# Kernel optimization log

Measured on AMD Instinct MI355X. Metric: run time of the kernel, lower is better.

The kernel has to match this reference:

```python
import jax, jax.numpy as jnp
import numpy as np

D_MODEL = 2048
NUM_HEADS = 32
NUM_KV_HEADS = 8
HEAD_DIM = D_MODEL // NUM_HEADS  # 64
KV_GROUPS = NUM_HEADS // NUM_KV_HEADS  # 4


def setup_inputs() -> dict:
    key = jax.random.key(0)
    k1, k2, k3, k4, k5 = jax.random.split(key, 5)
    scale = 0.02
    h_bsd = jax.random.normal(k1, (2, 2048, D_MODEL), dtype=jnp.float32)
    # nn.Linear weights stored as [out_features, in_features]
    w_q = jax.random.normal(k2, (NUM_HEADS * HEAD_DIM, D_MODEL), dtype=jnp.float32) * scale
    w_k = jax.random.normal(k3, (NUM_KV_HEADS * HEAD_DIM, D_MODEL), dtype=jnp.float32) * scale
    w_v = jax.random.normal(k4, (NUM_KV_HEADS * HEAD_DIM, D_MODEL), dtype=jnp.float32) * scale
    w_o = jax.random.normal(k5, (D_MODEL, NUM_HEADS * HEAD_DIM), dtype=jnp.float32) * scale
    return {"h_bsd": h_bsd, "w_q": w_q, "w_k": w_k, "w_v": w_v, "w_o": w_o}


def reference(h_bsd, w_q, w_k, w_v, w_o):
    b, s, _ = h_bsd.shape
    # projections (Linear without bias: x @ W.T)
    q = (h_bsd @ w_q.T).reshape(b, s, NUM_HEADS, HEAD_DIM).transpose(0, 2, 1, 3)      # [b, nq, s, h]
    k = (h_bsd @ w_k.T).reshape(b, s, NUM_KV_HEADS, HEAD_DIM).transpose(0, 2, 1, 3)   # [b, nkv, l, h]
    v = (h_bsd @ w_v.T).reshape(b, s, NUM_KV_HEADS, HEAD_DIM).transpose(0, 2, 1, 3)   # [b, nkv, l, h]
    # repeat_interleave over head dim to expand kv heads to query heads
    k = jnp.repeat(k, KV_GROUPS, axis=1)  # [b, nq, l, h]
    v = jnp.repeat(v, KV_GROUPS, axis=1)
    attn = jnp.einsum('bqsh,bqlh->bqsl', q, k) / jnp.sqrt(jnp.float32(HEAD_DIM))
    attn = jax.nn.softmax(attn, axis=-1)
    out = jnp.einsum('bqsl,bqlh->bqsh', attn, v)            # [b, nq, s, h]
    out = out.transpose(0, 2, 1, 3).reshape(b, s, D_MODEL)  # [b, s, d]
    return out @ w_o.T
```

## Files before the change

### kernel.cpp

```cpp
#include <hip/hip_runtime.h>
#include <stdint.h>

typedef unsigned short ushort_t;
typedef __attribute__((ext_vector_type(8))) short short8;
typedef __attribute__((ext_vector_type(4))) float floatx4;


__device__ __forceinline__ ushort_t f2bf(float f) {
  unsigned int u = __builtin_bit_cast(unsigned int, f);
  u += 0x7fffu + ((u >> 16) & 1u);
  return (ushort_t)(u >> 16);
}

__device__ __forceinline__ void gld16(const void* g, void* l) {
  __builtin_amdgcn_global_load_lds(
      (__attribute__((address_space(1))) void*)(void*)(g),
      (__attribute__((address_space(3))) void*)(l), 16, 0, 0);
}


__global__ __launch_bounds__(256)
void cast_all_kernel(const float* __restrict__ h, const float* __restrict__ wq,
                     const float* __restrict__ wk, const float* __restrict__ wv,
                     const float* __restrict__ wo,
                     ushort_t* __restrict__ h_bf, ushort_t* __restrict__ wqkv_bf,
                     ushort_t* __restrict__ wo_bf, float qscale) {
  long i = (long)blockIdx.x * 256 + threadIdx.x;
  const float4* src; ushort4* dst; float sc = 1.0f;
  if (i < 2097152L)       { src = (const float4*)h  + i;             dst = (ushort4*)h_bf + i; }
  else if (i < 3145728L)  { src = (const float4*)wq + (i - 2097152); dst = (ushort4*)wqkv_bf + (i - 2097152); sc = qscale; }
  else if (i < 3407872L)  { src = (const float4*)wk + (i - 3145728); dst = (ushort4*)wqkv_bf + (i - 3145728) + 1048576; }
  else if (i < 3670016L)  { src = (const float4*)wv + (i - 3407872); dst = (ushort4*)wqkv_bf + (i - 3407872) + 1310720; }
  else                    { src = (const float4*)wo + (i - 3670016); dst = (ushort4*)wo_bf + (i - 3670016); }
  float4 v = *src; ushort4 o;
  o.x = f2bf(v.x * sc); o.y = f2bf(v.y * sc);
  o.z = f2bf(v.z * sc); o.w = f2bf(v.w * sc);
  *dst = o;
}


template <int OM>
__global__ __launch_bounds__(256)
void gemm_bt(const ushort_t* __restrict__ A, const ushort_t* __restrict__ B,
             void* __restrict__ Cp, int M, int N, int K) {
  __shared__ ushort_t As[128 * 32];
  __shared__ ushort_t Bs[128 * 32];
  const int tid  = threadIdx.x;
  const int wave = tid >> 6, lane = tid & 63;
  const int quad = lane >> 4, l16 = lane & 15;
  const int wm = (wave >> 1) * 64, wn = (wave & 1) * 64;
  const int bm = blockIdx.x * 128, bn = blockIdx.y * 128;
  const int srow = lane >> 2, scc = lane & 3;

  floatx4 acc[4][4] = {};

  for (int k0 = 0; k0 < K; k0 += 32) {
#pragma unroll
    for (int r = 0; r < 2; ++r) {
      int c   = wave * 2 + r;
      int row = c * 16 + srow;
      int g   = scc ^ ((row >> 1) & 3);
      gld16(A + (long)(bm + row) * K + k0 + g * 8, As + c * 512 + lane * 8);
      gld16(B + (long)(bn + row) * K + k0 + g * 8, Bs + c * 512 + lane * 8);
    }
    __syncthreads();

    short8 af[4], bf[4];
#pragma unroll
    for (int i = 0; i < 4; ++i) {
      int m = wm + i * 16 + l16;
      af[i] = *(const short8*)(As + m * 32 + ((quad ^ ((m >> 1) & 3)) * 8));
      int n = wn + i * 16 + l16;
      bf[i] = *(const short8*)(Bs + n * 32 + ((quad ^ ((n >> 1) & 3)) * 8));
    }
#pragma unroll
    for (int i = 0; i < 4; ++i)
#pragma unroll
      for (int j = 0; j < 4; ++j)
        acc[i][j] = __builtin_amdgcn_mfma_f32_16x16x32_bf16(af[i], bf[j], acc[i][j], 0, 0, 0);
    __syncthreads();
  }

#pragma unroll
  for (int i = 0; i < 4; ++i)
#pragma unroll
    for (int j = 0; j < 4; ++j)
#pragma unroll
      for (int r = 0; r < 4; ++r) {
        int row = bm + wm + i * 16 + quad * 4 + r;
        int col = bn + wn + j * 16 + l16;
        if (OM == 0) ((ushort_t*)Cp)[(long)row * N + col] = f2bf(acc[i][j][r]);
        else         ((float*)Cp)[(long)row * N + col]    = acc[i][j][r];
      }
}


__global__ __launch_bounds__(256)
void transpose_v(const ushort_t* __restrict__ QKV, ushort_t* __restrict__ Vtg) {
  __shared__ ushort_t t[64 * 72];
  const int tid = threadIdx.x;
  const int b = blockIdx.z, kvh = blockIdx.y, l0 = blockIdx.x * 64;
#pragma unroll
  for (int r = 0; r < 2; ++r) {
    int idx = tid + r * 256;
    int row = idx >> 3, sub = idx & 7;
    short8 v = *(const short8*)(QKV + (long)(b * 2048 + l0 + row) * 3072 + 2560 + kvh * 64 + sub * 8);
    *(short8*)(t + row * 72 + sub * 8) = v;
  }
  __syncthreads();
#pragma unroll
  for (int r = 0; r < 2; ++r) {
    int idx = tid + r * 256;
    int hd = idx >> 3, sub = idx & 7;
    short8 o;
#pragma unroll
    for (int e = 0; e < 8; ++e) o[e] = (short)t[(sub * 8 + e) * 72 + hd];
    *(short8*)(Vtg + (long)((b * 8 + kvh) * 64 + hd) * 2048 + l0 + sub * 8) = o;
  }
}


__global__ __launch_bounds__(256, 4)
void attn_kernel(const ushort_t* __restrict__ QKV, const ushort_t* __restrict__ Vtg,
                 ushort_t* __restrict__ AO) {
  __shared__ ushort_t Ks[2][64 * 64];
  __shared__ ushort_t Vt[2][64 * 64];
  __shared__ ushort_t Pt[128 * 32];

  const int tid  = threadIdx.x;
  const int wave = tid >> 6, lane = tid & 63;
  const int quad = lane >> 4, l16 = lane & 15;
  const int b = blockIdx.z, h = blockIdx.y;
  const int q0 = blockIdx.x * 128;
  const int kvh = h >> 2;
  const long tok0 = (long)b * 2048 + q0;

  short8 qf[2][2];
#pragma unroll
  for (int kb = 0; kb < 2; ++kb)
#pragma unroll
    for (int j = 0; j < 2; ++j)
      qf[kb][j] = *(const short8*)(QKV + (tok0 + wave * 32 + j * 16 + l16) * 3072
                                   + h * 64 + kb * 32 + quad * 8);

  floatx4 oacc[2][4] = {};
  floatx4 osum[2] = {};

  short8 bones;
#pragma unroll
  for (int e = 0; e < 8; ++e) bones[e] = (short)0x3F80;

  const int lr = lane >> 3, sub = lane & 7;
  const int g = sub ^ lr;
  const ushort_t* Kbase = QKV + (long)b * 2048 * 3072 + 2048 + kvh * 64;
  const ushort_t* Vbase = Vtg + (long)(b * 8 + kvh) * 64 * 2048;

  auto stage = [&](int bf_, int l0) {
#pragma unroll
    for (int r = 0; r < 2; ++r) {
      int c = wave * 2 + r;
      int row = c * 8 + lr;
      gld16(Kbase + (long)(l0 + row) * 3072 + g * 8, Ks[bf_] + c * 512 + lane * 8);
      gld16(Vbase + (long)row * 2048 + l0 + g * 8, Vt[bf_] + c * 512 + lane * 8);
    }
  };

  stage(0, 0);

  for (int it = 0; it < 32; ++it) {
    __syncthreads();
    if (it + 1 < 32) stage((it + 1) & 1, (it + 1) * 64);
    const ushort_t* Kc = Ks[it & 1];
    const ushort_t* Vc = Vt[it & 1];

    floatx4 s[4][2] = {};
#pragma unroll
    for (int kb = 0; kb < 2; ++kb) {
      short8 kf[4];
#pragma unroll
      for (int i = 0; i < 4; ++i)
        kf[i] = *(const short8*)(Kc + (i * 16 + l16) * 64 + (((kb * 4 + quad) ^ (l16 & 7)) * 8));
#pragma unroll
      for (int i = 0; i < 4; ++i)
#pragma unroll
        for (int j = 0; j < 2; ++j)
          s[i][j] = __builtin_amdgcn_mfma_f32_16x16x32_bf16(kf[i], qf[kb][j], s[i][j], 0, 0, 0);
    }

#pragma unroll
    for (int hh = 0; hh < 2; ++hh) {
#pragma unroll
      for (int ii = 0; ii < 2; ++ii) {
        int i = hh * 2 + ii;
#pragma unroll
        for (int j = 0; j < 2; ++j) {
          float p0 = __builtin_amdgcn_exp2f(s[i][j][0]);
          float p1 = __builtin_amdgcn_exp2f(s[i][j][1]);
          float p2 = __builtin_amdgcn_exp2f(s[i][j][2]);
          float p3 = __builtin_amdgcn_exp2f(s[i][j][3]);
          uint2 w;
          w.x = __builtin_amdgcn_perm(__builtin_bit_cast(unsigned int, p1),
                                      __builtin_bit_cast(unsigned int, p0), 0x07060302u);
          w.y = __builtin_amdgcn_perm(__builtin_bit_cast(unsigned int, p3),
                                      __builtin_bit_cast(unsigned int, p2), 0x07060302u);
          int q = wave * 32 + j * 16 + l16;
          int c = ii * 2 + (quad >> 1);
          int idx = q * 32 + ((c ^ (l16 & 3)) * 8) + (quad & 1) * 4;
          *(uint2*)(Pt + idx) = w;
        }
      }
      short8 pf[2], vf[4];
#pragma unroll
      for (int im = 0; im < 2; ++im)
        pf[im] = *(const short8*)(Pt + (wave * 32 + im * 16 + l16) * 32
                                  + ((quad ^ (l16 & 3)) * 8));
#pragma unroll
      for (int n = 0; n < 4; ++n)
        vf[n] = *(const short8*)(Vc + (n * 16 + l16) * 64
                                 + (((hh * 4 + quad) ^ (l16 & 7)) * 8));
#pragma unroll
      for (int im = 0; im < 2; ++im) {
#pragma unroll
        for (int n = 0; n < 4; ++n)
          oacc[im][n] = __builtin_amdgcn_mfma_f32_16x16x32_bf16(pf[im], vf[n], oacc[im][n], 0, 0, 0);
        osum[im] = __builtin_amdgcn_mfma_f32_16x16x32_bf16(pf[im], bones, osum[im], 0, 0, 0);
      }
    }
  }

#pragma unroll
  for (int im = 0; im < 2; ++im) {
    floatx4 inv;
#pragma unroll
    for (int r = 0; r < 4; ++r) inv[r] = 1.0f / osum[im][r];
#pragma unroll
    for (int n = 0; n < 4; ++n)
#pragma unroll
      for (int r = 0; r < 4; ++r) {
        long t = tok0 + wave * 32 + im * 16 + quad * 4 + r;
        AO[t * 2048 + h * 64 + n * 16 + l16] = f2bf(oacc[im][n][r] * inv[r]);
      }
  }
}


extern "C" void kernel_launch(void* const* d_in, const int* in_sizes, int n_in,
                              void* d_out, int out_size, void* d_ws, size_t ws_size,
                              hipStream_t stream) {
  const float* h  = (const float*)d_in[0];
  const float* wq = (const float*)d_in[1];
  const float* wk = (const float*)d_in[2];
  const float* wv = (const float*)d_in[3];
  const float* wo = (const float*)d_in[4];
  float* out = (float*)d_out;

  const int BS = 4096, D = 2048, KV = 512, NQKV = 3072;

  ushort_t* h_bf    = (ushort_t*)d_ws;
  ushort_t* wqkv_bf = h_bf + (long)BS * D;
  ushort_t* wo_bf   = wqkv_bf + (long)NQKV * D;
  ushort_t* QKV     = wo_bf + (long)D * D;
  ushort_t* Vtg     = QKV + (long)BS * NQKV;
  ushort_t* AO      = h_bf;

  const float qscale = 0.125f * 1.44269504088896f;

  cast_all_kernel<<<4718592 / 256, 256, 0, stream>>>(h, wq, wk, wv, wo,
                                                     h_bf, wqkv_bf, wo_bf, qscale);

  gemm_bt<0><<<dim3(BS / 128, NQKV / 128), 256, 0, stream>>>(h_bf, wqkv_bf, QKV, BS, NQKV, D);

  transpose_v<<<dim3(32, 8, 2), 256, 0, stream>>>(QKV, Vtg);

  attn_kernel<<<dim3(2048 / 128, 32, 2), 256, 0, stream>>>(QKV, Vtg, AO);

  gemm_bt<1><<<dim3(BS / 128, D / 128), 256, 0, stream>>>(AO, wo_bf, out, BS, D, D);
}
```

Baseline: 320.9 us.

## Deepen GEMM K-tile to 64 and double attention query tile to 256 rows

Result: faster. 292.4 us (-8.9%).

```diff
diff --git a/kernel.cpp b/kernel.cpp
--- a/kernel.cpp
+++ b/kernel.cpp
@@ -43,41 +43,44 @@
 __global__ __launch_bounds__(256)
 void gemm_bt(const ushort_t* __restrict__ A, const ushort_t* __restrict__ B,
              void* __restrict__ Cp, int M, int N, int K) {
-  __shared__ ushort_t As[128 * 32];
-  __shared__ ushort_t Bs[128 * 32];
+  __shared__ ushort_t As[128 * 64];
+  __shared__ ushort_t Bs[128 * 64];
   const int tid  = threadIdx.x;
   const int wave = tid >> 6, lane = tid & 63;
   const int quad = lane >> 4, l16 = lane & 15;
   const int wm = (wave >> 1) * 64, wn = (wave & 1) * 64;
   const int bm = blockIdx.x * 128, bn = blockIdx.y * 128;
-  const int srow = lane >> 2, scc = lane & 3;
+  const int srow8 = lane >> 3, sub = lane & 7;
+  const int g = sub ^ srow8;
 
   floatx4 acc[4][4] = {};
 
-  for (int k0 = 0; k0 < K; k0 += 32) {
-#pragma unroll
-    for (int r = 0; r < 2; ++r) {
-      int c   = wave * 2 + r;
-      int row = c * 16 + srow;
-      int g   = scc ^ ((row >> 1) & 3);
+  for (int k0 = 0; k0 < K; k0 += 64) {
+#pragma unroll
+    for (int r = 0; r < 4; ++r) {
+      int c   = wave * 4 + r;
+      int row = c * 8 + srow8;
       gld16(A + (long)(bm + row) * K + k0 + g * 8, As + c * 512 + lane * 8);
       gld16(B + (long)(bn + row) * K + k0 + g * 8, Bs + c * 512 + lane * 8);
     }
     __syncthreads();
 
-    short8 af[4], bf[4];
-#pragma unroll
-    for (int i = 0; i < 4; ++i) {
-      int m = wm + i * 16 + l16;
-      af[i] = *(const short8*)(As + m * 32 + ((quad ^ ((m >> 1) & 3)) * 8));
-      int n = wn + i * 16 + l16;
-      bf[i] = *(const short8*)(Bs + n * 32 + ((quad ^ ((n >> 1) & 3)) * 8));
-    }
-#pragma unroll
-    for (int i = 0; i < 4; ++i)
-#pragma unroll
-      for (int j = 0; j < 4; ++j)
-        acc[i][j] = __builtin_amdgcn_mfma_f32_16x16x32_bf16(af[i], bf[j], acc[i][j], 0, 0, 0);
+#pragma unroll
+    for (int ks = 0; ks < 2; ++ks) {
+      short8 af[4], bf[4];
+#pragma unroll
+      for (int i = 0; i < 4; ++i) {
+        int m = wm + i * 16 + l16;
+        af[i] = *(const short8*)(As + m * 64 + (((ks * 4 + quad) ^ (m & 7)) * 8));
+        int n = wn + i * 16 + l16;
+        bf[i] = *(const short8*)(Bs + n * 64 + (((ks * 4 + quad) ^ (n & 7)) * 8));
+      }
+#pragma unroll
+      for (int i = 0; i < 4; ++i)
+#pragma unroll
+        for (int j = 0; j < 4; ++j)
+          acc[i][j] = __builtin_amdgcn_mfma_f32_16x16x32_bf16(af[i], bf[j], acc[i][j], 0, 0, 0);
+    }
     __syncthreads();
   }
 
@@ -120,18 +123,18 @@
 }
 
 
-__global__ __launch_bounds__(256, 4)
+__global__ __launch_bounds__(512, 4)
 void attn_kernel(const ushort_t* __restrict__ QKV, const ushort_t* __restrict__ Vtg,
                  ushort_t* __restrict__ AO) {
   __shared__ ushort_t Ks[2][64 * 64];
   __shared__ ushort_t Vt[2][64 * 64];
-  __shared__ ushort_t Pt[128 * 32];
+  __shared__ ushort_t Pt[256 * 68];
 
   const int tid  = threadIdx.x;
   const int wave = tid >> 6, lane = tid & 63;
   const int quad = lane >> 4, l16 = lane & 15;
   const int b = blockIdx.z, h = blockIdx.y;
-  const int q0 = blockIdx.x * 128;
+  const int q0 = blockIdx.x * 256;
   const int kvh = h >> 2;
   const long tok0 = (long)b * 2048 + q0;
 
@@ -156,13 +159,9 @@
   const ushort_t* Vbase = Vtg + (long)(b * 8 + kvh) * 64 * 2048;
 
   auto stage = [&](int bf_, int l0) {
-#pragma unroll
-    for (int r = 0; r < 2; ++r) {
-      int c = wave * 2 + r;
-      int row = c * 8 + lr;
-      gld16(Kbase + (long)(l0 + row) * 3072 + g * 8, Ks[bf_] + c * 512 + lane * 8);
-      gld16(Vbase + (long)row * 2048 + l0 + g * 8, Vt[bf_] + c * 512 + lane * 8);
-    }
+    int row = wave * 8 + lr;
+    gld16(Kbase + (long)(l0 + row) * 3072 + g * 8, Ks[bf_] + wave * 512 + lane * 8);
+    gld16(Vbase + (long)row * 2048 + l0 + g * 8, Vt[bf_] + wave * 512 + lane * 8);
   };
 
   stage(0, 0);
@@ -188,36 +187,34 @@
     }
 
 #pragma unroll
-    for (int hh = 0; hh < 2; ++hh) {
-#pragma unroll
-      for (int ii = 0; ii < 2; ++ii) {
-        int i = hh * 2 + ii;
-#pragma unroll
-        for (int j = 0; j < 2; ++j) {
-          float p0 = __builtin_amdgcn_exp2f(s[i][j][0]);
-          float p1 = __builtin_amdgcn_exp2f(s[i][j][1]);
-          float p2 = __builtin_amdgcn_exp2f(s[i][j][2]);
-          float p3 = __builtin_amdgcn_exp2f(s[i][j][3]);
-          uint2 w;
-          w.x = __builtin_amdgcn_perm(__builtin_bit_cast(unsigned int, p1),
-                                      __builtin_bit_cast(unsigned int, p0), 0x07060302u);
-          w.y = __builtin_amdgcn_perm(__builtin_bit_cast(unsigned int, p3),
-                                      __builtin_bit_cast(unsigned int, p2), 0x07060302u);
-          int q = wave * 32 + j * 16 + l16;
-          int c = ii * 2 + (quad >> 1);
-          int idx = q * 32 + ((c ^ (l16 & 3)) * 8) + (quad & 1) * 4;
-          *(uint2*)(Pt + idx) = w;
-        }
-      }
+    for (int i = 0; i < 4; ++i)
+#pragma unroll
+      for (int j = 0; j < 2; ++j) {
+        float p0 = __builtin_amdgcn_exp2f(s[i][j][0]);
+        float p1 = __builtin_amdgcn_exp2f(s[i][j][1]);
+        float p2 = __builtin_amdgcn_exp2f(s[i][j][2]);
+        float p3 = __builtin_amdgcn_exp2f(s[i][j][3]);
+        uint2 w;
+        w.x = __builtin_amdgcn_perm(__builtin_bit_cast(unsigned int, p1),
+                                    __builtin_bit_cast(unsigned int, p0), 0x07060302u);
+        w.y = __builtin_amdgcn_perm(__builtin_bit_cast(unsigned int, p3),
+                                    __builtin_bit_cast(unsigned int, p2), 0x07060302u);
+        int q = wave * 32 + j * 16 + l16;
+        int idx = q * 68 + (((i * 2 + (quad >> 1)) ^ (l16 & 7)) * 8) + (quad & 1) * 4;
+        *(uint2*)(Pt + idx) = w;
+      }
+
+#pragma unroll
+    for (int kb = 0; kb < 2; ++kb) {
       short8 pf[2], vf[4];
 #pragma unroll
       for (int im = 0; im < 2; ++im)
-        pf[im] = *(const short8*)(Pt + (wave * 32 + im * 16 + l16) * 32
-                                  + ((quad ^ (l16 & 3)) * 8));
+        pf[im] = *(const short8*)(Pt + (wave * 32 + im * 16 + l16) * 68
+                                  + (((kb * 4 + quad) ^ (l16 & 7)) * 8));
 #pragma unroll
       for (int n = 0; n < 4; ++n)
         vf[n] = *(const short8*)(Vc + (n * 16 + l16) * 64
-                                 + (((hh * 4 + quad) ^ (l16 & 7)) * 8));
+                                 + (((kb * 4 + quad) ^ (l16 & 7)) * 8));
 #pragma unroll
       for (int im = 0; im < 2; ++im) {
 #pragma unroll
@@ -272,7 +269,7 @@
 
   transpose_v<<<dim3(32, 8, 2), 256, 0, stream>>>(QKV, Vtg);
 
-  attn_kernel<<<dim3(2048 / 128, 32, 2), 256, 0, stream>>>(QKV, Vtg, AO);
+  attn_kernel<<<dim3(2048 / 256, 32, 2), 512, 0, stream>>>(QKV, Vtg, AO);
 
   gemm_bt<1><<<dim3(BS / 128, D / 128), 256, 0, stream>>>(AO, wo_bf, out, BS, D, D);
 }
```
